# Kernel optimization log

Hardware: AMD Instinct MI355X
Metric: run time of the kernel (lower is better)

Reference implementation:

```python
import jax, jax.numpy as jnp
import numpy as np

N_IMG = 512
N_ANGLES = 180


def _bilinear(img, sy, sx):
    """Bilinear sample img at float coords (sy, sx); zero outside the image."""
    n = img.shape[0]
    y0 = jnp.floor(sy)
    x0 = jnp.floor(sx)
    wy = sy - y0
    wx = sx - x0
    y0i = y0.astype(jnp.int32)
    x0i = x0.astype(jnp.int32)

    def gather(yi, xi):
        valid = (yi >= 0) & (yi < n) & (xi >= 0) & (xi < n)
        yc = jnp.clip(yi, 0, n - 1)
        xc = jnp.clip(xi, 0, n - 1)
        return jnp.where(valid, img[yc, xc], jnp.zeros((), img.dtype))

    v00 = gather(y0i, x0i)
    v01 = gather(y0i, x0i + 1)
    v10 = gather(y0i + 1, x0i)
    v11 = gather(y0i + 1, x0i + 1)
    return (v00 * (1 - wy) * (1 - wx) + v01 * (1 - wy) * wx
            + v10 * wy * (1 - wx) + v11 * wy * wx)


def _radon(img, angles):
    """skimage-style radon: rotate image by each angle, sum along axis 0.
    Returns sinogram of shape (n_detectors, n_angles) = (N, len(angles))."""
    n = img.shape[0]
    c = (n - 1) * 0.5  # rotation about image center
    coords = jnp.arange(n, dtype=img.dtype) - c
    yc, xc = jnp.meshgrid(coords, coords, indexing="ij")  # (N, N)

    def one_angle(theta_deg):
        t = jnp.deg2rad(theta_deg.astype(img.dtype))
        co, si = jnp.cos(t), jnp.sin(t)
        # inverse-rotation sampling coordinates (CCW rotation of the image)
        sx = co * xc + si * yc + c
        sy = -si * xc + co * yc + c
        rotated = _bilinear(img, sy, sx)  # (N, N)
        return rotated.sum(axis=0)        # projection along detector rows -> (N,)

    sino = jax.vmap(one_angle)(angles)  # (n_angles, N)
    return sino.T                        # (N, n_angles)


def setup_inputs() -> dict:
    key = jax.random.key(0)
    img = jax.random.uniform(key, (N_IMG, N_IMG), dtype=jnp.float32)  # nonnegative PET activity
    angles = jnp.arange(N_ANGLES, dtype=jnp.int32)  # degrees 0..179 (skimage default)
    return {"img": img, "angles": angles}


def reference(img, angles):
    return _radon(img, angles)
```

## Files before the change

kernel.cpp:

```cpp
#include <hip/hip_runtime.h>
#include <hip/hip_fp16.h>
#include <stdint.h>

#define N 512
#define NA 180
#define TD 64
#define TW 96
#define TILE_DW (36 * 256)
#define PP 708
#define PR 704
#define POFF 96

#define WS_IMGPB  0
#define WS_IMGTPB (PR * PP)
#define WS_TAB    (2 * PR * PP)
#define WS_FLAGS  (WS_TAB + 4 * NA)

typedef _Float16 hh2 __attribute__((ext_vector_type(2)));
union H2U { uint32_t u; hh2 h; };

__device__ __forceinline__ hh2 cvt_pkrtz(float a, float b) {
    return __builtin_bit_cast(hh2, __builtin_amdgcn_cvt_pkrtz(a, b));
}

__device__ __forceinline__ void load16_to_lds(const uint32_t* g, uint32_t* l) {
    __builtin_amdgcn_global_load_lds(
        (const __attribute__((address_space(1))) void*)g,
        (__attribute__((address_space(3))) void*)l,
        16 , 0 , 0 );
}

__global__ __launch_bounds__(256) void pad_kernel(const float* __restrict__ img,
                                                  const int* __restrict__ angles,
                                                  uint32_t* __restrict__ imgPB,
                                                  uint32_t* __restrict__ imgTPB,
                                                  float4* __restrict__ tab,
                                                  int* __restrict__ flags) {
    __shared__ float lds[33 * 34];
    const int tid = threadIdx.x;
    const int bx = blockIdx.x, by = blockIdx.y;

    if (bx == 0 && by == 0 && tid < NA) {
        float t = (float)angles[tid] * 0.017453292519943295f;
        float si = sinf(t), co = cosf(t);
        int useT = fabsf(si) > fabsf(co);
        float4 e;
        if (useT) { e.x = co; e.y = -si; e.z = si; e.w = co; }
        else      { e.x = si; e.y = co;  e.z = co; e.w = -si; }
        tab[tid] = e;
        flags[tid] = useT;
    }

    for (int idx = tid; idx < 33 * 33; idx += 256) {
        int r = idx / 33, cc = idx - r * 33;
        int y = by * 32 + r - POFF, x = bx * 32 + cc - POFF;
        bool in = ((unsigned)y < N) && ((unsigned)x < N);
        lds[r * 34 + cc] = in ? img[y * N + x] : 0.0f;
    }
    __syncthreads();
    const int r0 = tid >> 5, cl = tid & 31;
#pragma unroll
    for (int j = 0; j < 4; ++j) {
        int row = j * 8 + r0;
        float v0 = lds[row * 34 + cl], v1 = lds[row * 34 + cl + 1];
        __half2 h = __halves2half2(__float2half(v0), __float2half(v1));
        imgPB[(size_t)(by * 32 + row) * PP + bx * 32 + cl] = *(uint32_t*)&h;
        float t0 = lds[cl * 34 + row], t1 = lds[(cl + 1) * 34 + row];
        __half2 ht = __halves2half2(__float2half(t0), __float2half(t1));
        imgTPB[(size_t)(bx * 32 + row) * PP + by * 32 + cl] = *(uint32_t*)&ht;
    }
}

__global__ __launch_bounds__(512, 4) void radon_kernel(const uint32_t* __restrict__ imgPB,
                                                       const uint32_t* __restrict__ imgTPB,
                                                       const float4* __restrict__ tab,
                                                       const int* __restrict__ flags,
                                                       float* __restrict__ out) {
    __shared__ uint32_t tile[2 * TILE_DW];

    const int tid  = threadIdx.x;
    const int lane = tid & 63;
    const int wave = tid >> 6;
    const int d0 = blockIdx.x * TD;
    const int a  = blockIdx.y;

    const float c = 255.5f;
    const float4 tb = tab[a];
    const float au = tb.x, bus = tb.y, av = tb.z, bvs = tb.w;

    const float xc0 = (float)d0 - c, xc1 = (float)(d0 + TD - 1) - c;
    const float buA = fmaf(bus, xc0, c), buB = fmaf(bus, xc1, c);
    const float bvA = fmaf(bvs, xc0, c), bvB = fmaf(bvs, xc1, c);
    const float buMin = fminf(buA, buB), buMax = fmaxf(buA, buB);
    const float bvMin = fminf(bvA, bvB), bvMax = fmaxf(bvA, bvB);

    const uint32_t* __restrict__ src = flags[a] ? imgTPB : imgPB;

    const float xcl = (float)(d0 + lane) - c;
    const float buLb = fmaf(bus, xcl, c);
    const float bvLb = fmaf(bvs, xcl, c);

    const int t0g  = wave * 256 + (lane << 2);
    const int q0   = t0g / TW;
    const int c0   = t0g - q0 * TW;
    const int goff0 = q0 * PP + c0;

    auto params = [&](int p, int& ub0, int& vb, int& nch) -> bool {
        const int ip = p * 64;
        const float fi0 = (float)ip - c, fi1 = (float)(ip + 63) - c;
        const float fiLoU = (au >= 0.0f) ? fi0 : fi1, fiHiU = (au >= 0.0f) ? fi1 : fi0;
        const float fiLoV = (av >= 0.0f) ? fi0 : fi1, fiHiV = (av >= 0.0f) ? fi1 : fi0;
        const float umin = fmaf(au, fiLoU, buMin), umax = fmaf(au, fiHiU, buMax);
        const float vmin = fmaf(av, fiLoV, bvMin), vmax = fmaf(av, fiHiV, bvMax);
        if (umin > (float)N || umax < -1.0f || vmin > (float)N || vmax < -1.0f)
            return false;
        ub0 = (((int)floorf(umin)) - 1) & ~3;
        vb  = ((int)floorf(vmin)) - 1;
        int rows = ((int)floorf(vmax)) + 3 - vb;
        nch = (rows * TW + 255) >> 8;
        return true;
    };

    auto stage = [&](int ub0, int vb, int nch, int base) {
        const uint32_t* gb = src + (vb + POFF) * PP + (ub0 + POFF) + goff0;
        int cc = c0;
#pragma unroll
        for (int st = 0; st < 5; ++st) {
            int chunk = st * 8 + wave;
            if (chunk < nch) load16_to_lds(gb, &tile[base + chunk * 256]);
            cc += 32;
            int wrap = (cc >= TW);
            cc = wrap ? cc - TW : cc;
            gb += 21 * PP + 32 + (wrap ? (PP - TW) : 0);
        }
    };

    float s = 0.0f;

    int pc = -1, ub0c = 0, vbc = 0, nchc = 0;
    for (int p = 0; p < 8; ++p) {
        if (params(p, ub0c, vbc, nchc)) { pc = p; break; }
    }

    int base = 0;
    if (pc >= 0) {
        stage(ub0c, vbc, nchc, base);
        __syncthreads();
    }
    while (pc >= 0) {
        int pn = -1, ub0n = 0, vbn = 0, nchn = 0;
        for (int p = pc + 1; p < 8; ++p) {
            if (params(p, ub0n, vbn, nchn)) { pn = p; break; }
        }
        if (pn >= 0) stage(ub0n, vbn, nchn, base ^ TILE_DW);

        {
            const float buL = buLb - (float)ub0c;
            const float bvL = bvLb - (float)vbc;
            const float fiw = (float)(pc * 64 + wave * 8) - c;
            float u = fmaf(au, fiw, buL);
            float v = fmaf(av, fiw, bvL);
            const uint32_t* tl = tile + base;
#pragma unroll
            for (int k = 0; k < 8; ++k) {
                float wx = __builtin_amdgcn_fractf(u);
                float wy = __builtin_amdgcn_fractf(v);
                int iu = (int)u, iv = (int)v;
                int ai = iv * TW + iu;
                H2U P0, P1;
                P0.u = tl[ai];
                P1.u = tl[ai + TW];
                hh2 wy2 = cvt_pkrtz(wy, wy);
                hh2 m   = wy2 * (P1.h - P0.h) + P0.h;
                hh2 wv  = cvt_pkrtz(1.0f - wx, wx);
                s = __builtin_amdgcn_fdot2(wv, m, s, false);
                u += au;
                v += av;
            }
        }
        __syncthreads();
        pc = pn; ub0c = ub0n; vbc = vbn; nchc = nchn;
        base ^= TILE_DW;
    }

    __syncthreads();
    float* ft = (float*)tile;
    ft[tid] = s;
    __syncthreads();
    if (tid < 64) {
        float r = ft[tid]       + ft[tid + 64]  + ft[tid + 128] + ft[tid + 192]
                + ft[tid + 256] + ft[tid + 320] + ft[tid + 384] + ft[tid + 448];
        out[(d0 + tid) * NA + a] = r;
    }
}

extern "C" void kernel_launch(void* const* d_in, const int* in_sizes, int n_in,
                              void* d_out, int out_size, void* d_ws, size_t ws_size,
                              hipStream_t stream) {
    const float* img  = (const float*)d_in[0];
    const int* angles = (const int*)d_in[1];
    float* out = (float*)d_out;
    float* ws  = (float*)d_ws;

    uint32_t* imgPB  = (uint32_t*)(ws + WS_IMGPB);
    uint32_t* imgTPB = (uint32_t*)(ws + WS_IMGTPB);
    float4*   tab    = (float4*)(ws + WS_TAB);
    int*      flags  = (int*)(ws + WS_FLAGS);

    dim3 pgrid(22, 22);
    pad_kernel<<<pgrid, 256, 0, stream>>>(img, angles, imgPB, imgTPB, tab, flags);

    dim3 grid(N / TD, NA);
    radon_kernel<<<grid, 512, 0, stream>>>(imgPB, imgTPB, tab, flags, out);
}
```

Before: 94.00 us.

## Replace LDS tile staging with direct global gathers and analytic ray clipping

Drops the double-buffered LDS tile pipeline, which used async global-to-LDS loads and per-chunk barriers. Each thread now gathers directly from the padded fp16 image in global memory, relying on L2/cache. The packed layout changes from horizontal pairs to vertical pairs, so each sample needs two adjacent dword loads. Per-thread loop bounds are computed analytically from the image extent, so out-of-image samples are skipped. The trade-off is uncoalesced global gathers instead of LDS reads, with fewer threads per block and no staging overhead.

```diff
diff --git a/kernel.cpp b/kernel.cpp
--- a/kernel.cpp
+++ b/kernel.cpp
@@ -4,15 +4,12 @@
 
 #define N 512
 #define NA 180
-#define TD 64
-#define TW 96
-#define TILE_DW (36 * 256)
 #define PP 708
 #define PR 704
 #define POFF 96
 
-#define WS_IMGPB  0
-#define WS_IMGTPB (PR * PP)
+#define WS_IMGVP  0
+#define WS_IMGVPT (PR * PP)
 #define WS_TAB    (2 * PR * PP)
 #define WS_FLAGS  (WS_TAB + 4 * NA)
 
@@ -23,17 +20,10 @@
     return __builtin_bit_cast(hh2, __builtin_amdgcn_cvt_pkrtz(a, b));
 }
 
-__device__ __forceinline__ void load16_to_lds(const uint32_t* g, uint32_t* l) {
-    __builtin_amdgcn_global_load_lds(
-        (const __attribute__((address_space(1))) void*)g,
-        (__attribute__((address_space(3))) void*)l,
-        16 , 0 , 0 );
-}
-
 __global__ __launch_bounds__(256) void pad_kernel(const float* __restrict__ img,
                                                   const int* __restrict__ angles,
-                                                  uint32_t* __restrict__ imgPB,
-                                                  uint32_t* __restrict__ imgTPB,
+                                                  uint32_t* __restrict__ imgVP,
+                                                  uint32_t* __restrict__ imgVPT,
                                                   float4* __restrict__ tab,
                                                   int* __restrict__ flags) {
     __shared__ float lds[33 * 34];
@@ -62,134 +52,91 @@
 #pragma unroll
     for (int j = 0; j < 4; ++j) {
         int row = j * 8 + r0;
-        float v0 = lds[row * 34 + cl], v1 = lds[row * 34 + cl + 1];
+        float v0 = lds[row * 34 + cl], v1 = lds[(row + 1) * 34 + cl];
         __half2 h = __halves2half2(__float2half(v0), __float2half(v1));
-        imgPB[(size_t)(by * 32 + row) * PP + bx * 32 + cl] = *(uint32_t*)&h;
-        float t0 = lds[cl * 34 + row], t1 = lds[(cl + 1) * 34 + row];
+        imgVP[(size_t)(by * 32 + row) * PP + bx * 32 + cl] = *(uint32_t*)&h;
+        float t0 = lds[cl * 34 + row], t1 = lds[cl * 34 + row + 1];
         __half2 ht = __halves2half2(__float2half(t0), __float2half(t1));
-        imgTPB[(size_t)(bx * 32 + row) * PP + by * 32 + cl] = *(uint32_t*)&ht;
+        imgVPT[(size_t)(bx * 32 + row) * PP + by * 32 + cl] = *(uint32_t*)&ht;
     }
 }
 
-__global__ __launch_bounds__(512, 4) void radon_kernel(const uint32_t* __restrict__ imgPB,
-                                                       const uint32_t* __restrict__ imgTPB,
-                                                       const float4* __restrict__ tab,
-                                                       const int* __restrict__ flags,
-                                                       float* __restrict__ out) {
-    __shared__ uint32_t tile[2 * TILE_DW];
+__global__ __launch_bounds__(256) void radon_kernel(const uint32_t* __restrict__ imgVP,
+                                                    const uint32_t* __restrict__ imgVPT,
+                                                    const float4* __restrict__ tab,
+                                                    const int* __restrict__ flags,
+                                                    float* __restrict__ out) {
+    __shared__ float red[256];
 
-    const int tid  = threadIdx.x;
-    const int lane = tid & 63;
-    const int wave = tid >> 6;
-    const int d0 = blockIdx.x * TD;
-    const int a  = blockIdx.y;
+    const int tid = threadIdx.x;
+    const int dl  = tid & 63;
+    const int q   = tid >> 6;
+    const int d0  = blockIdx.x * 64;
+    const int a   = blockIdx.y;
 
     const float c = 255.5f;
     const float4 tb = tab[a];
     const float au = tb.x, bus = tb.y, av = tb.z, bvs = tb.w;
+    const uint32_t* __restrict__ src = flags[a] ? imgVPT : imgVP;
 
-    const float xc0 = (float)d0 - c, xc1 = (float)(d0 + TD - 1) - c;
-    const float buA = fmaf(bus, xc0, c), buB = fmaf(bus, xc1, c);
-    const float bvA = fmaf(bvs, xc0, c), bvB = fmaf(bvs, xc1, c);
-    const float buMin = fminf(buA, buB), buMax = fmaxf(buA, buB);
-    const float bvMin = fminf(bvA, bvB), bvMax = fmaxf(bvA, bvB);
+    const float xcl = (float)(d0 + dl) - c;
+    const float buP = fmaf(bus, xcl, c + (float)POFF) - au * c;
+    const float bvP = fmaf(bvs, xcl, c + (float)POFF) - av * c;
 
-    const uint32_t* __restrict__ src = flags[a] ? imgTPB : imgPB;
+    int iLo = q * 128, iHi = q * 128 + 127;
+    if (fabsf(au) > 1e-6f) {
+        float ia = 1.0f / au;
+        float t0 = (94.0f - buP) * ia, t1 = (609.0f - buP) * ia;
+        float lo = fminf(t0, t1), hi = fmaxf(t0, t1);
+        iLo = max(iLo, (int)ceilf(lo));
+        iHi = min(iHi, (int)floorf(hi));
+    } else if (buP < 94.0f || buP > 609.0f) {
+        iHi = iLo - 1;
+    }
+    if (fabsf(av) > 1e-6f) {
+        float ia = 1.0f / av;
+        float t0 = (94.0f - bvP) * ia, t1 = (609.0f - bvP) * ia;
+        float lo = fminf(t0, t1), hi = fmaxf(t0, t1);
+        iLo = max(iLo, (int)ceilf(lo));
+        iHi = min(iHi, (int)floorf(hi));
+    } else if (bvP < 94.0f || bvP > 609.0f) {
+        iHi = iLo - 1;
+    }
 
-    const float xcl = (float)(d0 + lane) - c;
-    const float buLb = fmaf(bus, xcl, c);
-    const float bvLb = fmaf(bvs, xcl, c);
-
-    const int t0g  = wave * 256 + (lane << 2);
-    const int q0   = t0g / TW;
-    const int c0   = t0g - q0 * TW;
-    const int goff0 = q0 * PP + c0;
-
-    auto params = [&](int p, int& ub0, int& vb, int& nch) -> bool {
-        const int ip = p * 64;
-        const float fi0 = (float)ip - c, fi1 = (float)(ip + 63) - c;
-        const float fiLoU = (au >= 0.0f) ? fi0 : fi1, fiHiU = (au >= 0.0f) ? fi1 : fi0;
-        const float fiLoV = (av >= 0.0f) ? fi0 : fi1, fiHiV = (av >= 0.0f) ? fi1 : fi0;
-        const float umin = fmaf(au, fiLoU, buMin), umax = fmaf(au, fiHiU, buMax);
-        const float vmin = fmaf(av, fiLoV, bvMin), vmax = fmaf(av, fiHiV, bvMax);
-        if (umin > (float)N || umax < -1.0f || vmin > (float)N || vmax < -1.0f)
-            return false;
-        ub0 = (((int)floorf(umin)) - 1) & ~3;
-        vb  = ((int)floorf(vmin)) - 1;
-        int rows = ((int)floorf(vmax)) + 3 - vb;
-        nch = (rows * TW + 255) >> 8;
-        return true;
+    float s = 0.0f;
+    float fi = (float)iLo;
+    auto sample = [&]() {
+        float u = fmaf(au, fi, buP);
+        float v = fmaf(av, fi, bvP);
+        float wx = __builtin_amdgcn_fractf(u);
+        float wy = __builtin_amdgcn_fractf(v);
+        int iu = (int)u, iv = (int)v;
+        const uint32_t* p = src + iv * PP + iu;
+        H2U P0, P1;
+        P0.u = p[0];
+        P1.u = p[1];
+        hh2 wyv = cvt_pkrtz(1.0f - wy, wy);
+        float mx0 = __builtin_amdgcn_fdot2(wyv, P0.h, 0.0f, false);
+        float mx1 = __builtin_amdgcn_fdot2(wyv, P1.h, 0.0f, false);
+        s = fmaf(wx, mx1 - mx0, s + mx0);
+        fi += 1.0f;
     };
 
-    auto stage = [&](int ub0, int vb, int nch, int base) {
-        const uint32_t* gb = src + (vb + POFF) * PP + (ub0 + POFF) + goff0;
-        int cc = c0;
+    if (iHi >= iLo) {
+        const int cnt = iHi - iLo + 1;
+        const int n4  = cnt >> 2;
+        for (int it = 0; it < n4; ++it) {
 #pragma unroll
-        for (int st = 0; st < 5; ++st) {
-            int chunk = st * 8 + wave;
-            if (chunk < nch) load16_to_lds(gb, &tile[base + chunk * 256]);
-            cc += 32;
-            int wrap = (cc >= TW);
-            cc = wrap ? cc - TW : cc;
-            gb += 21 * PP + 32 + (wrap ? (PP - TW) : 0);
+            for (int k = 0; k < 4; ++k) sample();
         }
-    };
-
-    float s = 0.0f;
-
-    int pc = -1, ub0c = 0, vbc = 0, nchc = 0;
-    for (int p = 0; p < 8; ++p) {
-        if (params(p, ub0c, vbc, nchc)) { pc = p; break; }
+        const int rem = cnt & 3;
+        for (int r2 = 0; r2 < rem; ++r2) sample();
     }
 
-    int base = 0;
-    if (pc >= 0) {
-        stage(ub0c, vbc, nchc, base);
-        __syncthreads();
-    }
-    while (pc >= 0) {
-        int pn = -1, ub0n = 0, vbn = 0, nchn = 0;
-        for (int p = pc + 1; p < 8; ++p) {
-            if (params(p, ub0n, vbn, nchn)) { pn = p; break; }
-        }
-        if (pn >= 0) stage(ub0n, vbn, nchn, base ^ TILE_DW);
-
-        {
-            const float buL = buLb - (float)ub0c;
-            const float bvL = bvLb - (float)vbc;
-            const float fiw = (float)(pc * 64 + wave * 8) - c;
-            float u = fmaf(au, fiw, buL);
-            float v = fmaf(av, fiw, bvL);
-            const uint32_t* tl = tile + base;
-#pragma unroll
-            for (int k = 0; k < 8; ++k) {
-                float wx = __builtin_amdgcn_fractf(u);
-                float wy = __builtin_amdgcn_fractf(v);
-                int iu = (int)u, iv = (int)v;
-                int ai = iv * TW + iu;
-                H2U P0, P1;
-                P0.u = tl[ai];
-                P1.u = tl[ai + TW];
-                hh2 wy2 = cvt_pkrtz(wy, wy);
-                hh2 m   = wy2 * (P1.h - P0.h) + P0.h;
-                hh2 wv  = cvt_pkrtz(1.0f - wx, wx);
-                s = __builtin_amdgcn_fdot2(wv, m, s, false);
-                u += au;
-                v += av;
-            }
-        }
-        __syncthreads();
-        pc = pn; ub0c = ub0n; vbc = vbn; nchc = nchn;
-        base ^= TILE_DW;
-    }
-
-    __syncthreads();
-    float* ft = (float*)tile;
-    ft[tid] = s;
+    red[tid] = s;
     __syncthreads();
     if (tid < 64) {
-        float r = ft[tid]       + ft[tid + 64]  + ft[tid + 128] + ft[tid + 192]
-                + ft[tid + 256] + ft[tid + 320] + ft[tid + 384] + ft[tid + 448];
+        float r = red[tid] + red[tid + 64] + red[tid + 128] + red[tid + 192];
         out[(d0 + tid) * NA + a] = r;
     }
 }
@@ -202,14 +149,14 @@
     float* out = (float*)d_out;
     float* ws  = (float*)d_ws;
 
-    uint32_t* imgPB  = (uint32_t*)(ws + WS_IMGPB);
-    uint32_t* imgTPB = (uint32_t*)(ws + WS_IMGTPB);
+    uint32_t* imgVP  = (uint32_t*)(ws + WS_IMGVP);
+    uint32_t* imgVPT = (uint32_t*)(ws + WS_IMGVPT);
     float4*   tab    = (float4*)(ws + WS_TAB);
     int*      flags  = (int*)(ws + WS_FLAGS);
 
     dim3 pgrid(22, 22);
-    pad_kernel<<<pgrid, 256, 0, stream>>>(img, angles, imgPB, imgTPB, tab, flags);
+    pad_kernel<<<pgrid, 256, 0, stream>>>(img, angles, imgVP, imgVPT, tab, flags);
 
-    dim3 grid(N / TD, NA);
-    radon_kernel<<<grid, 512, 0, stream>>>(imgPB, imgTPB, tab, flags, out);
+    dim3 grid(N / 64, NA);
+    radon_kernel<<<grid, 256, 0, stream>>>(imgVP, imgVPT, tab, flags, out);
 }
```

New measurement: 101.5 us. 1.08x slower.

## Fully unroll phase pipeline with unconditional staging and rotated phase order

Applied to the files above, without the earlier changes.

Replaces the data-dependent while loop over the eight 64-row phases with a fully unrolled loop. Every phase is now staged, with clamped addresses and a fixed 40-chunk tile, and explicit vmcnt waits plus raw barriers replace __syncthreads. The phase order is rotated per block so blocks spread their global reads across different image regions. This removes branchy scheduling and lets loads stay in flight across iterations. In exchange it loads tiles for dead phases and enlarges the LDS tiles, which may lower occupancy.

```diff
diff --git a/kernel.cpp b/kernel.cpp
--- a/kernel.cpp
+++ b/kernel.cpp
@@ -6,7 +6,8 @@
 #define NA 180
 #define TD 64
 #define TW 96
-#define TILE_DW (36 * 256)
+#define NCH 40
+#define TILE_DW (NCH * 256)
 #define PP 708
 #define PR 704
 #define POFF 96
@@ -21,6 +22,11 @@
 
 __device__ __forceinline__ hh2 cvt_pkrtz(float a, float b) {
     return __builtin_bit_cast(hh2, __builtin_amdgcn_cvt_pkrtz(a, b));
+}
+
+__device__ __forceinline__ uint32_t packh2(float a, float b) {
+    __half2 h = __halves2half2(__float2half(a), __float2half(b));
+    return *(uint32_t*)&h;
 }
 
 __device__ __forceinline__ void load16_to_lds(const uint32_t* g, uint32_t* l) {
@@ -62,12 +68,10 @@
 #pragma unroll
     for (int j = 0; j < 4; ++j) {
         int row = j * 8 + r0;
-        float v0 = lds[row * 34 + cl], v1 = lds[row * 34 + cl + 1];
-        __half2 h = __halves2half2(__float2half(v0), __float2half(v1));
-        imgPB[(size_t)(by * 32 + row) * PP + bx * 32 + cl] = *(uint32_t*)&h;
-        float t0 = lds[cl * 34 + row], t1 = lds[(cl + 1) * 34 + row];
-        __half2 ht = __halves2half2(__float2half(t0), __float2half(t1));
-        imgTPB[(size_t)(bx * 32 + row) * PP + by * 32 + cl] = *(uint32_t*)&ht;
+        imgPB[(size_t)(by * 32 + row) * PP + bx * 32 + cl] =
+            packh2(lds[row * 34 + cl], lds[row * 34 + cl + 1]);
+        imgTPB[(size_t)(bx * 32 + row) * PP + by * 32 + cl] =
+            packh2(lds[cl * 34 + row], lds[(cl + 1) * 34 + row]);
     }
 }
 
@@ -83,6 +87,7 @@
     const int wave = tid >> 6;
     const int d0 = blockIdx.x * TD;
     const int a  = blockIdx.y;
+    const int rot = (blockIdx.x + blockIdx.y) & 7;
 
     const float c = 255.5f;
     const float4 tb = tab[a];
@@ -105,29 +110,30 @@
     const int c0   = t0g - q0 * TW;
     const int goff0 = q0 * PP + c0;
 
-    auto params = [&](int p, int& ub0, int& vb, int& nch) -> bool {
-        const int ip = p * 64;
+    int ub0s[8], vbs[8], lives[8];
+#pragma unroll
+    for (int p8 = 0; p8 < 8; ++p8) {
+        const int ph = (p8 + rot) & 7;
+        const int ip = ph * 64;
         const float fi0 = (float)ip - c, fi1 = (float)(ip + 63) - c;
         const float fiLoU = (au >= 0.0f) ? fi0 : fi1, fiHiU = (au >= 0.0f) ? fi1 : fi0;
         const float fiLoV = (av >= 0.0f) ? fi0 : fi1, fiHiV = (av >= 0.0f) ? fi1 : fi0;
         const float umin = fmaf(au, fiLoU, buMin), umax = fmaf(au, fiHiU, buMax);
         const float vmin = fmaf(av, fiLoV, bvMin), vmax = fmaf(av, fiHiV, bvMax);
-        if (umin > (float)N || umax < -1.0f || vmin > (float)N || vmax < -1.0f)
-            return false;
-        ub0 = (((int)floorf(umin)) - 1) & ~3;
-        vb  = ((int)floorf(vmin)) - 1;
-        int rows = ((int)floorf(vmax)) + 3 - vb;
-        nch = (rows * TW + 255) >> 8;
-        return true;
-    };
-
-    auto stage = [&](int ub0, int vb, int nch, int base) {
-        const uint32_t* gb = src + (vb + POFF) * PP + (ub0 + POFF) + goff0;
+        lives[p8] = !(umin > (float)N || umax < -1.0f || vmin > (float)N || vmax < -1.0f);
+        int ub0 = (((int)floorf(fminf(umin, 1e6f))) - 1) & ~3;
+        int vb  = ((int)floorf(fminf(vmin, 1e6f))) - 1;
+        ub0s[p8] = min(max(ub0, -96), 516);
+        vbs[p8]  = min(max(vb, -96), 501);
+    }
+
+    auto stageTo = [&](int p8, int base) {
+        const uint32_t* gb = src + (vbs[p8] + POFF) * PP + (ub0s[p8] + POFF) + goff0;
+        uint32_t* lb = &tile[base];
         int cc = c0;
 #pragma unroll
         for (int st = 0; st < 5; ++st) {
-            int chunk = st * 8 + wave;
-            if (chunk < nch) load16_to_lds(gb, &tile[base + chunk * 256]);
+            load16_to_lds(gb, lb + (st * 8 + wave) * 256);
             cc += 32;
             int wrap = (cc >= TW);
             cc = wrap ? cc - TW : cc;
@@ -137,27 +143,19 @@
 
     float s = 0.0f;
 
-    int pc = -1, ub0c = 0, vbc = 0, nchc = 0;
-    for (int p = 0; p < 8; ++p) {
-        if (params(p, ub0c, vbc, nchc)) { pc = p; break; }
-    }
-
-    int base = 0;
-    if (pc >= 0) {
-        stage(ub0c, vbc, nchc, base);
-        __syncthreads();
-    }
-    while (pc >= 0) {
-        int pn = -1, ub0n = 0, vbn = 0, nchn = 0;
-        for (int p = pc + 1; p < 8; ++p) {
-            if (params(p, ub0n, vbn, nchn)) { pn = p; break; }
-        }
-        if (pn >= 0) stage(ub0n, vbn, nchn, base ^ TILE_DW);
-
-        {
-            const float buL = buLb - (float)ub0c;
-            const float bvL = bvLb - (float)vbc;
-            const float fiw = (float)(pc * 64 + wave * 8) - c;
+    stageTo(0, 0);
+#pragma unroll
+    for (int p8 = 0; p8 < 8; ++p8) {
+        const int base = (p8 & 1) * TILE_DW;
+        if (p8 < 7) stageTo(p8 + 1, base ^ TILE_DW);
+        if (p8 < 7) { asm volatile("s_waitcnt vmcnt(5)" ::: "memory"); }
+        else        { asm volatile("s_waitcnt vmcnt(0)" ::: "memory"); }
+        __builtin_amdgcn_s_barrier();
+        if (lives[p8]) {
+            const int ph = (p8 + rot) & 7;
+            const float buL = buLb - (float)ub0s[p8];
+            const float bvL = bvLb - (float)vbs[p8];
+            const float fiw = (float)(ph * 64 + wave * 8) - c;
             float u = fmaf(au, fiw, buL);
             float v = fmaf(av, fiw, bvL);
             const uint32_t* tl = tile + base;
@@ -178,12 +176,9 @@
                 v += av;
             }
         }
-        __syncthreads();
-        pc = pn; ub0c = ub0n; vbc = vbn; nchc = nchn;
-        base ^= TILE_DW;
-    }
-
-    __syncthreads();
+        __builtin_amdgcn_s_barrier();
+    }
+
     float* ft = (float*)tile;
     ft[tid] = s;
     __syncthreads();
```

Result: no change. 92.66 us (-1.4%).
